# Kernel tuning notes

Measured on AMD Instinct MI355X. Metric: run time of the kernel, lower is better.

The kernel has to match this reference:

```python
import jax, jax.numpy as jnp
import numpy as np

B, IN = 8192, 8000
C, S, O = 16, 500, 64          # num_chunks, chunk_size, fc_repr_dim
F = C * O                       # fc_0_out_feat = 1024
E, D, T = 8, 512, 2            # num_experts, fc_task_dim, num_tasks
NC = (32, 2)                    # num_classes per task
EPS = 1e-5


def _bn(h, g, b, axis):
    # training-mode BatchNorm1d: biased variance over the batch axis
    m = h.mean(axis=axis, keepdims=True)
    v = h.var(axis=axis, keepdims=True)
    return (h - m) * jax.lax.rsqrt(v + EPS) * g + b


def _swish(x):
    return x * jax.nn.sigmoid(x)


def setup_inputs() -> dict:
    key = jax.random.key(0)
    ks = jax.random.split(key, 10)
    s = 0.02
    return {
        "x": jax.random.normal(ks[0], (B, IN), dtype=jnp.float32),
        "w0": jax.random.normal(ks[1], (C, O, S), dtype=jnp.float32) * s,
        "b0": jnp.zeros((F,), jnp.float32),
        "bn0_g": jnp.ones((F,), jnp.float32),
        "bn0_b": jnp.zeros((F,), jnp.float32),
        "gate_w": jax.random.normal(ks[2], (T, F, E), dtype=jnp.float32) * s,
        "gate_b": jnp.zeros((T, E), jnp.float32),
        "exp_w": jax.random.normal(ks[3], (E, F, D), dtype=jnp.float32) * s,
        "exp_bn_g": jnp.ones((E, D), jnp.float32),
        "exp_bn_b": jnp.zeros((E, D), jnp.float32),
        "task_w": jax.random.normal(ks[4], (T, D, D), dtype=jnp.float32) * s,
        "task_bn_g": jnp.ones((T, D), jnp.float32),
        "task_bn_b": jnp.zeros((T, D), jnp.float32),
        "fin_w_a": jax.random.normal(ks[5], (D, NC[0]), dtype=jnp.float32) * s,
        "fin_b_a": jnp.zeros((NC[0],), jnp.float32),
        "fin_w_b": jax.random.normal(ks[6], (D, NC[1]), dtype=jnp.float32) * s,
        "fin_b_b": jnp.zeros((NC[1],), jnp.float32),
    }


def reference(x, w0, b0, bn0_g, bn0_b, gate_w, gate_b, exp_w, exp_bn_g,
              exp_bn_b, task_w, task_bn_g, task_bn_b, fin_w_a, fin_b_a,
              fin_w_b, fin_b_b):
    b = x.shape[0]
    # SplitLinear: block-diagonal linear over C chunks of size S -> O each
    h0 = jnp.einsum('bcs,cos->bco', x.reshape(b, C, S), w0).reshape(b, F) + b0
    h0 = _swish(_bn(h0, bn0_g, bn0_b, axis=0))                  # [B, F]
    # per-task gates with softmax over experts
    gates = jax.nn.softmax(
        jnp.einsum('bf,tfe->tbe', h0, gate_w) + gate_b[:, None, :], axis=-1)
    # expert branches: Linear(no bias) + BN + Swish, vectorized over experts
    eh = jnp.einsum('bf,efd->bed', h0, exp_w)                   # [B, E, D]
    eh = _swish(_bn(eh, exp_bn_g, exp_bn_b, axis=0))
    # gate-weighted sum over experts, per task
    mix = jnp.einsum('tbe,bed->tbd', gates, eh)                 # [T, B, D]
    # task branches: Linear(no bias) + BN + Swish
    th = jnp.einsum('tbd,tdk->tbk', mix, task_w)
    th = _swish(_bn(th, task_bn_g[:, None, :], task_bn_b[:, None, :], axis=1))
    out_a = th[0] @ fin_w_a + fin_b_a                           # [B, 32]
    out_b = th[1] @ fin_w_b + fin_b_b                           # [B, 2]
    return jnp.concatenate([out_a, out_b], axis=1)             # [B, 34]
```

## Files before the change

kernel.cpp:

```cpp
#include <hip/hip_runtime.h>
#include <math.h>

#define B_ 8192
#define IN_ 8000
#define C_ 16
#define S_ 500
#define O_ 64
#define F_ 1024
#define E_ 8
#define D_ 512
#define T_ 2
#define OUTW 34
#define EPS_ 1e-5f

typedef __attribute__((ext_vector_type(8))) short bf16x8;
typedef __attribute__((ext_vector_type(4))) float f32x4;

__device__ __forceinline__ float swishf(float x) {
    return x / (1.0f + __expf(-x));
}

__device__ __forceinline__ unsigned short f2bf(float f) {
    union { float f; unsigned u; } c;
    c.f = f;
    unsigned r = c.u + 0x7fffu + ((c.u >> 16) & 1u);
    return (unsigned short)(r >> 16);
}
__device__ __forceinline__ float bf2f(unsigned short b) {
    union { unsigned u; float f; } c;
    c.u = ((unsigned)b) << 16;
    return c.f;
}

__device__ __forceinline__ void gld16(const void* g, void* l) {
    __builtin_amdgcn_global_load_lds(
        (const __attribute__((address_space(1))) void*)g,
        (__attribute__((address_space(3))) void*)l, 16, 0, 0);
}

__global__ __launch_bounds__(256) void k_split(const float* __restrict__ x,
                                               const float* __restrict__ w0,
                                               const float* __restrict__ b0,
                                               unsigned short* __restrict__ h0raw,
                                               float* __restrict__ psum,
                                               float* __restrict__ psq) {
    __shared__ __align__(16) unsigned short As[128 * 72];
    __shared__ __align__(16) unsigned short Bs[64 * 72];
    int tid = threadIdx.x;
    int c = blockIdx.y;
    int brow0 = blockIdx.x * 128;
    const float* xp = x + (size_t)brow0 * IN_ + c * S_;
    const float* wp = w0 + (size_t)c * O_ * S_;

    int w = tid >> 6, lane = tid & 63;
    int l15 = lane & 15, quad = lane >> 4;
    int wm = w * 32;

    f32x4 acc[2][4] = {};

    for (int k0 = 0; k0 < 512; k0 += 64) {
#pragma unroll
        for (int i = 0; i < 8; i++) {
            int li = tid + i * 256;
            int row = li >> 4, c4 = li & 15;
            int gk = k0 + c4 * 4;
            float4 v = make_float4(0.f, 0.f, 0.f, 0.f);
            if (gk + 3 < S_) v = *(const float4*)(xp + (size_t)row * IN_ + gk);
            unsigned short u[4] = { f2bf(v.x), f2bf(v.y), f2bf(v.z), f2bf(v.w) };
            *(ushort4*)&As[row * 72 + c4 * 4] = *(ushort4*)u;
        }
#pragma unroll
        for (int i = 0; i < 4; i++) {
            int li = tid + i * 256;
            int row = li >> 4, c4 = li & 15;
            int gk = k0 + c4 * 4;
            float4 v = make_float4(0.f, 0.f, 0.f, 0.f);
            if (gk + 3 < S_) v = *(const float4*)(wp + (size_t)row * S_ + gk);
            unsigned short u[4] = { f2bf(v.x), f2bf(v.y), f2bf(v.z), f2bf(v.w) };
            *(ushort4*)&Bs[row * 72 + c4 * 4] = *(ushort4*)u;
        }
        __syncthreads();
#pragma unroll
        for (int kk = 0; kk < 64; kk += 32) {
            bf16x8 af[2], wf[4];
#pragma unroll
            for (int i = 0; i < 2; i++)
                af[i] = *(const bf16x8*)&As[(wm + i * 16 + l15) * 72 + kk + quad * 8];
#pragma unroll
            for (int j = 0; j < 4; j++)
                wf[j] = *(const bf16x8*)&Bs[(j * 16 + l15) * 72 + kk + quad * 8];
#pragma unroll
            for (int i = 0; i < 2; i++)
#pragma unroll
                for (int j = 0; j < 4; j++)
                    acc[i][j] = __builtin_amdgcn_mfma_f32_16x16x32_bf16(af[i], wf[j], acc[i][j], 0, 0, 0);
        }
        __syncthreads();
    }

    int colbase = c * O_;
    float sj[4], qj[4];
#pragma unroll
    for (int j = 0; j < 4; j++) {
        int col = j * 16 + l15;
        float bb = b0[colbase + col];
        float s = 0.f, q = 0.f;
#pragma unroll
        for (int i = 0; i < 2; i++) {
#pragma unroll
            for (int reg = 0; reg < 4; reg++) {
                float v = acc[i][j][reg] + bb;
                int rl = wm + i * 16 + quad * 4 + reg;
                h0raw[(size_t)(brow0 + rl) * F_ + colbase + col] = f2bf(v);
                s += v; q += v * v;
            }
        }
        s += __shfl_down(s, 32, 64); s += __shfl_down(s, 16, 64);
        q += __shfl_down(q, 32, 64); q += __shfl_down(q, 16, 64);
        sj[j] = s; qj[j] = q;
    }
    __syncthreads();
    float* red = (float*)As;
    if (lane < 16) {
#pragma unroll
        for (int j = 0; j < 4; j++) {
            int col = j * 16 + l15;
            red[col * 4 + w] = sj[j];
            red[256 + col * 4 + w] = qj[j];
        }
    }
    __syncthreads();
    if (tid < 64) {
        float ss = red[tid * 4] + red[tid * 4 + 1] + red[tid * 4 + 2] + red[tid * 4 + 3];
        float qq = red[256 + tid * 4] + red[256 + tid * 4 + 1] + red[256 + tid * 4 + 2] + red[256 + tid * 4 + 3];
        size_t idx = (size_t)blockIdx.x * F_ + colbase + tid;
        psum[idx] = ss; psq[idx] = qq;
    }
}

__global__ __launch_bounds__(64) void k_stats_b(const float* __restrict__ psum,
                                                const float* __restrict__ psq,
                                                int N, int YS,
                                                const float* __restrict__ g,
                                                const float* __restrict__ beta,
                                                unsigned long long gslab,
                                                float* __restrict__ scale,
                                                float* __restrict__ shift,
                                                unsigned long long oslab) {
    int n = blockIdx.x * 64 + threadIdx.x;
    int z = blockIdx.z;
    float s = 0.f, q = 0.f;
    for (int y = 0; y < YS; y++) {
        size_t idx = ((size_t)(z * YS + y)) * N + n;
        s += psum[idx]; q += psq[idx];
    }
    float mean = s * (1.0f / B_);
    float var = q * (1.0f / B_) - mean * mean;
    float sc = g[z * gslab + n] * rsqrtf(var + EPS_);
    scale[z * oslab + n] = sc;
    shift[z * oslab + n] = beta[z * gslab + n] - mean * sc;
}

__global__ __launch_bounds__(256) void k_wt2(const float* __restrict__ exp_w,
                                             unsigned short* __restrict__ wtE,
                                             const float* __restrict__ task_w,
                                             unsigned short* __restrict__ twt) {
    int z = blockIdx.z;
    const float* ip; unsigned short* op; int K, N;
    if (z < 8) {
        K = F_; N = D_;
        ip = exp_w + (size_t)z * K * N;
        op = wtE + (size_t)z * N * K;
    } else {
        if (blockIdx.x >= 16) return;
        K = D_; N = D_;
        int zz = z - 8;
        ip = task_w + (size_t)zz * K * N;
        op = twt + (size_t)zz * N * K;
    }
    __shared__ float t[32][33];
    int k0 = blockIdx.x * 32, n0 = blockIdx.y * 32;
    int tn = threadIdx.x & 31, tk = threadIdx.x >> 5;
#pragma unroll
    for (int p = 0; p < 4; p++) {
        int k = tk + p * 8;
        t[k][tn] = ip[(size_t)(k0 + k) * N + n0 + tn];
    }
    __syncthreads();
    int tk2 = threadIdx.x & 31, tn2 = threadIdx.x >> 5;
#pragma unroll
    for (int p = 0; p < 4; p++) {
        int n = tn2 + p * 8;
        op[(size_t)(n0 + n) * K + k0 + tk2] = f2bf(t[tk2][n]);
    }
}

__global__ __launch_bounds__(512) void k_bng(const unsigned short* __restrict__ h0,
                                             const float* __restrict__ scale,
                                             const float* __restrict__ shift,
                                             const float* __restrict__ gate_w,
                                             const float* __restrict__ gate_b,
                                             unsigned short* __restrict__ h0bf,
                                             float* __restrict__ gates) {
    __shared__ __align__(16) unsigned short gwt[16 * 1032];
    __shared__ __align__(16) unsigned short As[32 * 1032];
    __shared__ float plog[4][32][16];
    int tid = threadIdx.x;
    int brow = blockIdx.x * 32;
    for (int idx = tid; idx < 16 * 1024; idx += 512) {
        int col = idx >> 10, f = idx & 1023;
        int t = col >> 3, e = col & 7;
        gwt[col * 1032 + f] = f2bf(gate_w[(size_t)t * (F_ * E_) + (size_t)f * E_ + e]);
    }
    int f0 = (tid & 255) * 4;
    int rh = tid >> 8;
    float4 sc4 = *(const float4*)(scale + f0);
    float4 sh4 = *(const float4*)(shift + f0);
    float scv[4] = { sc4.x, sc4.y, sc4.z, sc4.w };
    float shv[4] = { sh4.x, sh4.y, sh4.z, sh4.w };
#pragma unroll
    for (int r = 0; r < 16; r++) {
        int row = rh * 16 + r;
        ushort4 u = *(const ushort4*)(h0 + (size_t)(brow + row) * F_ + f0);
        unsigned short uu[4] = { u.x, u.y, u.z, u.w };
        unsigned short ov[4];
#pragma unroll
        for (int j = 0; j < 4; j++)
            ov[j] = f2bf(swishf(scv[j] * bf2f(uu[j]) + shv[j]));
        *(ushort4*)(h0bf + (size_t)(brow + row) * F_ + f0) = *(ushort4*)ov;
        *(ushort4*)&As[row * 1032 + f0] = *(ushort4*)ov;
    }
    __syncthreads();
    int w = tid >> 6, lane = tid & 63;
    int l15 = lane & 15, quad = lane >> 4;
    int slot = w & 1, kq = w >> 1;
    f32x4 acc = {};
    const unsigned short* ap = &As[(slot * 16 + l15) * 1032 + kq * 256 + quad * 8];
    const unsigned short* wp = &gwt[l15 * 1032 + kq * 256 + quad * 8];
#pragma unroll
    for (int k0 = 0; k0 < 256; k0 += 32) {
        bf16x8 af = *(const bf16x8*)(ap + k0);
        bf16x8 wf = *(const bf16x8*)(wp + k0);
        acc = __builtin_amdgcn_mfma_f32_16x16x32_bf16(af, wf, acc, 0, 0, 0);
    }
#pragma unroll
    for (int reg = 0; reg < 4; reg++)
        plog[kq][slot * 16 + quad * 4 + reg][l15] = acc[reg];
    __syncthreads();
    if (tid < 32) {
        int r = tid;
        float lg[16];
#pragma unroll
        for (int c = 0; c < 16; c++)
            lg[c] = plog[0][r][c] + plog[1][r][c] + plog[2][r][c] + plog[3][r][c] + gate_b[c];
#pragma unroll
        for (int t = 0; t < 2; t++) {
            float mx = -1e30f;
#pragma unroll
            for (int e = 0; e < 8; e++) mx = fmaxf(mx, lg[t * 8 + e]);
            float ex[8], s = 0.f;
#pragma unroll
            for (int e = 0; e < 8; e++) { ex[e] = __expf(lg[t * 8 + e] - mx); s += ex[e]; }
            float inv = 1.0f / s;
#pragma unroll
            for (int e = 0; e < 8; e++)
                gates[(size_t)t * (B_ * E_) + (size_t)(brow + r) * E_ + e] = ex[e] * inv;
        }
    }
}

__global__ __launch_bounds__(256) void k_gemm_bf16(const unsigned short* __restrict__ A,
                                                   unsigned long long aslab,
                                                   const unsigned short* __restrict__ Wt,
                                                   unsigned long long wslab,
                                                   unsigned short* __restrict__ C,
                                                   unsigned long long cslab, int K,
                                                   float* __restrict__ psum,
                                                   float* __restrict__ psq) {
    __shared__ __align__(16) unsigned short As[128 * 32];
    __shared__ __align__(16) unsigned short Ws[128 * 32];
    int z = blockIdx.z;
    A  += (size_t)z * aslab;
    Wt += (size_t)z * wslab;
    C  += (size_t)z * cslab;
    const int N = gridDim.y * 128;
    int row0 = blockIdx.x * 128, col0 = blockIdx.y * 128;
    int tid = threadIdx.x;
    int w = tid >> 6, lane = tid & 63;
    int l15 = lane & 15, quad = lane >> 4;

    const unsigned short* ga0 = A  + (size_t)(row0 + w * 32 + (lane >> 2)) * K + (lane & 3) * 8;
    const unsigned short* ga1 = ga0 + 16 * (size_t)K;
    const unsigned short* gw0 = Wt + (size_t)(col0 + w * 32 + (lane >> 2)) * K + (lane & 3) * 8;
    const unsigned short* gw1 = gw0 + 16 * (size_t)K;
    unsigned short* la0 = As + (w * 32) * 32;
    unsigned short* la1 = As + (w * 32 + 16) * 32;
    unsigned short* lw0 = Ws + (w * 32) * 32;
    unsigned short* lw1 = Ws + (w * 32 + 16) * 32;

    int wm = (w & 1) * 64, wn = (w >> 1) * 64;
    const unsigned short* Afr = As + (size_t)(wm + l15) * 32 + quad * 8;
    const unsigned short* Wfr = Ws + (size_t)(wn + l15) * 32 + quad * 8;

    f32x4 acc[4][4] = {};

    for (int k0 = 0; k0 < K; k0 += 32) {
        gld16(ga0 + k0, la0);
        gld16(ga1 + k0, la1);
        gld16(gw0 + k0, lw0);
        gld16(gw1 + k0, lw1);
        __syncthreads();
        bf16x8 af[4], wf[4];
#pragma unroll
        for (int i = 0; i < 4; i++) af[i] = *(const bf16x8*)(Afr + i * 16 * 32);
#pragma unroll
        for (int j = 0; j < 4; j++) wf[j] = *(const bf16x8*)(Wfr + j * 16 * 32);
#pragma unroll
        for (int i = 0; i < 4; i++)
#pragma unroll
            for (int j = 0; j < 4; j++)
                acc[i][j] = __builtin_amdgcn_mfma_f32_16x16x32_bf16(af[i], wf[j], acc[i][j], 0, 0, 0);
        __syncthreads();
    }

#pragma unroll
    for (int i = 0; i < 4; i++) {
        int r = row0 + wm + i * 16 + quad * 4;
#pragma unroll
        for (int j = 0; j < 4; j++) {
            int cc = col0 + wn + j * 16 + l15;
            unsigned short* cp = C + (size_t)r * N + cc;
#pragma unroll
            for (int reg = 0; reg < 4; reg++)
                cp[(size_t)reg * N] = f2bf(acc[i][j][reg]);
        }
    }

    float* red = (float*)As;
    float sj[4], qj[4];
#pragma unroll
    for (int j = 0; j < 4; j++) {
        float s = 0.f, q = 0.f;
#pragma unroll
        for (int i = 0; i < 4; i++)
#pragma unroll
            for (int reg = 0; reg < 4; reg++) {
                float v = acc[i][j][reg];
                s += v; q += v * v;
            }
        s += __shfl_down(s, 32, 64); s += __shfl_down(s, 16, 64);
        q += __shfl_down(q, 32, 64); q += __shfl_down(q, 16, 64);
        sj[j] = s; qj[j] = q;
    }
    if (lane < 16) {
#pragma unroll
        for (int j = 0; j < 4; j++) {
            int cib = wn + j * 16 + lane;
            red[cib * 2 + (w & 1)] = sj[j];
            red[256 + cib * 2 + (w & 1)] = qj[j];
        }
    }
    __syncthreads();
    if (tid < 128) {
        float s = red[tid * 2] + red[tid * 2 + 1];
        float q = red[256 + tid * 2] + red[256 + tid * 2 + 1];
        size_t row = (size_t)z * gridDim.x + blockIdx.x;
        psum[row * N + col0 + tid] = s;
        psq[row * N + col0 + tid] = q;
    }
}

__global__ __launch_bounds__(512, 2) void k_gemm256(const unsigned short* __restrict__ A,
                                                    const unsigned short* __restrict__ Wt,
                                                    unsigned short* __restrict__ Cc,
                                                    int N, int K,
                                                    float* __restrict__ psum,
                                                    float* __restrict__ psq) {
    __shared__ __align__(16) unsigned short lds[2][2][2][8192];
    int tid = threadIdx.x;
    int w = tid >> 6, lane = tid & 63;
    int l15 = lane & 15, quad = lane >> 4;
    int wm = w >> 2, wn = w & 3;

    int lin = blockIdx.y * gridDim.x + blockIdx.x;
    int cpx = (gridDim.x * gridDim.y) >> 3;
    int swz = (lin & 7) * cpx + (lin >> 3);
    int bx = swz & (gridDim.x - 1), by = swz / gridDim.x;
    int row0 = bx * 256, col0 = by * 256;

    int srow = tid >> 3, sperm = (tid & 7) ^ (srow & 7);
    const unsigned short* pA = A  + (size_t)(row0 + srow) * K + sperm * 8;
    const unsigned short* pB = Wt + (size_t)(col0 + srow) * K + sperm * 8;

    int aoffs[2];
#pragma unroll
    for (int kk = 0; kk < 2; kk++)
        aoffs[kk] = l15 * 64 + ((kk * 4 + quad) ^ (l15 & 7)) * 8;

    f32x4 acc[8][4] = {};
    bf16x8 afr[4][2], bfr[2][2];
    int nt = K >> 6;

#define STAGE256(t1, nb) do {                                                              \
    const unsigned short* sA = pA + (size_t)(t1) * 64;                                     \
    const unsigned short* sB = pB + (size_t)(t1) * 64;                                     \
    _Pragma("unroll")                                                                      \
    for (int h = 0; h < 2; h++)                                                            \
        _Pragma("unroll")                                                                  \
        for (int L = 0; L < 2; L++) {                                                      \
            gld16(sA + (size_t)(h * 128 + L * 64) * K, &lds[nb][0][h][w * 512 + L * 4096]);\
            gld16(sB + (size_t)(h * 128 + L * 64) * K, &lds[nb][1][h][w * 512 + L * 4096]);\
        }                                                                                  \
} while (0)

#define LDA256(mh) do {                                                                    \
    _Pragma("unroll")                                                                      \
    for (int mf = 0; mf < 4; mf++)                                                         \
        _Pragma("unroll")                                                                  \
        for (int kk = 0; kk < 2; kk++)                                                     \
            afr[mf][kk] = *(const bf16x8*)(Ab + ((mh) * 4 + mf) * 1024 + aoffs[kk]);       \
} while (0)

#define LDB256(nh) do {                                                                    \
    _Pragma("unroll")                                                                      \
    for (int nf = 0; nf < 2; nf++)                                                         \
        _Pragma("unroll")                                                                  \
        for (int kk = 0; kk < 2; kk++)                                                     \
            bfr[nf][kk] = *(const bf16x8*)(Bb + ((nh) * 2 + nf) * 1024 + aoffs[kk]);       \
} while (0)

#define MMA256(mh, nh) do {                                                                \
    _Pragma("unroll")                                                                      \
    for (int mf = 0; mf < 4; mf++)                                                         \
        _Pragma("unroll")                                                                  \
        for (int nf = 0; nf < 2; nf++)                                                     \
            _Pragma("unroll")                                                              \
            for (int kk = 0; kk < 2; kk++)                                                 \
                acc[(mh) * 4 + mf][(nh) * 2 + nf] = __builtin_amdgcn_mfma_f32_16x16x32_bf16(\
                    afr[mf][kk], bfr[nf][kk], acc[(mh) * 4 + mf][(nh) * 2 + nf], 0, 0, 0); \
} while (0)

#define PHASE_MID()                                                                        \
    __builtin_amdgcn_s_barrier();                                                          \
    asm volatile("s_waitcnt lgkmcnt(0)" ::: "memory");                                     \
    __builtin_amdgcn_sched_barrier(0);                                                     \
    __builtin_amdgcn_s_setprio(1);

#define PHASE_END()                                                                        \
    __builtin_amdgcn_s_setprio(0);                                                         \
    __builtin_amdgcn_sched_barrier(0);                                                     \
    __builtin_amdgcn_s_barrier();

    STAGE256(0, 0);
    asm volatile("s_waitcnt vmcnt(0)" ::: "memory");
    __builtin_amdgcn_s_barrier();

    for (int t = 0; t < nt; t++) {
        int buf = t & 1;
        const unsigned short* Ab = &lds[buf][0][wm][0];
        const unsigned short* Bb = &lds[buf][1][wn >> 1][(wn & 1) * 4096];
        LDA256(0); LDB256(0);
        if (t + 1 < nt) STAGE256(t + 1, buf ^ 1);
        PHASE_MID();
        MMA256(0, 0);
        PHASE_END();
        LDB256(1);
        PHASE_MID();
        MMA256(0, 1);
        PHASE_END();
        LDA256(1);
        PHASE_MID();
        MMA256(1, 1);
        PHASE_END();
        LDB256(0);
        PHASE_MID();
        MMA256(1, 0);
        __builtin_amdgcn_s_setprio(0);
        __builtin_amdgcn_sched_barrier(0);
        asm volatile("s_waitcnt vmcnt(0)" ::: "memory");
        __builtin_amdgcn_s_barrier();
    }
#undef STAGE256
#undef LDA256
#undef LDB256
#undef MMA256
#undef PHASE_MID
#undef PHASE_END

    __syncthreads();

#pragma unroll
    for (int mf = 0; mf < 8; mf++) {
        int r = row0 + wm * 128 + mf * 16 + quad * 4;
#pragma unroll
        for (int nf = 0; nf < 4; nf++) {
            int cc = col0 + wn * 64 + nf * 16 + l15;
            unsigned short* cp = Cc + (size_t)r * N + cc;
#pragma unroll
            for (int reg = 0; reg < 4; reg++)
                cp[(size_t)reg * N] = f2bf(acc[mf][nf][reg]);
        }
    }

    float* red = (float*)&lds[0][0][0][0];
    float* redq = red + 512;
    float sj[4], qj[4];
#pragma unroll
    for (int nf = 0; nf < 4; nf++) {
        float s = 0.f, q = 0.f;
#pragma unroll
        for (int mf = 0; mf < 8; mf++)
#pragma unroll
            for (int reg = 0; reg < 4; reg++) {
                float v = acc[mf][nf][reg];
                s += v; q += v * v;
            }
        s += __shfl_down(s, 32, 64); s += __shfl_down(s, 16, 64);
        q += __shfl_down(q, 32, 64); q += __shfl_down(q, 16, 64);
        sj[nf] = s; qj[nf] = q;
    }
    if (quad == 0) {
#pragma unroll
        for (int nf = 0; nf < 4; nf++) {
            int cib = wn * 64 + nf * 16 + l15;
            red[cib * 2 + wm] = sj[nf];
            redq[cib * 2 + wm] = qj[nf];
        }
    }
    __syncthreads();
    if (tid < 256) {
        float s = red[tid * 2] + red[tid * 2 + 1];
        float q = redq[tid * 2] + redq[tid * 2 + 1];
        psum[(size_t)bx * N + col0 + tid] = s;
        psq [(size_t)bx * N + col0 + tid] = q;
    }
}

__global__ __launch_bounds__(256) void k_mix(const unsigned short* __restrict__ eh,
                                             const float* __restrict__ scale,
                                             const float* __restrict__ shift,
                                             const float* __restrict__ gates,
                                             unsigned short* __restrict__ mix) {
    __shared__ float scl[E_ * D_], shl[E_ * D_];
    __shared__ float gl[2][2][8];
    int tid = threadIdx.x;
#pragma unroll
    for (int i = 0; i < 4; i++) {
        int li = tid + i * 256;
        ((float4*)scl)[li] = ((const float4*)scale)[li];
        ((float4*)shl)[li] = ((const float4*)shift)[li];
    }
    if (tid < 32) {
        int sub = tid >> 4, t = (tid >> 3) & 1, e = tid & 7;
        gl[sub][t][e] = gates[(size_t)t * (B_ * E_) + (size_t)(blockIdx.x * 2 + sub) * E_ + e];
    }
    __syncthreads();
    int sub = tid >> 7;
    int b = blockIdx.x * 2 + sub;
    int d0 = (tid & 127) * 4;
    float a0[4] = {0.f, 0.f, 0.f, 0.f}, a1[4] = {0.f, 0.f, 0.f, 0.f};
#pragma unroll
    for (int e = 0; e < E_; e++) {
        ushort4 u = *(const ushort4*)&eh[(size_t)b * (E_ * D_) + e * D_ + d0];
        float4 sc4 = *(const float4*)&scl[e * D_ + d0];
        float4 sh4 = *(const float4*)&shl[e * D_ + d0];
        float g0 = gl[sub][0][e], g1 = gl[sub][1][e];
        unsigned short uu[4] = { u.x, u.y, u.z, u.w };
        float scv[4] = { sc4.x, sc4.y, sc4.z, sc4.w };
        float shv[4] = { sh4.x, sh4.y, sh4.z, sh4.w };
#pragma unroll
        for (int l = 0; l < 4; l++) {
            float sw = swishf(scv[l] * bf2f(uu[l]) + shv[l]);
            a0[l] += g0 * sw;
            a1[l] += g1 * sw;
        }
    }
    unsigned short o0[4], o1[4];
#pragma unroll
    for (int l = 0; l < 4; l++) { o0[l] = f2bf(a0[l]); o1[l] = f2bf(a1[l]); }
    *(ushort4*)&mix[(size_t)b * D_ + d0] = *(ushort4*)o0;
    *(ushort4*)&mix[(size_t)(B_ * D_) + (size_t)b * D_ + d0] = *(ushort4*)o1;
}

__global__ __launch_bounds__(256) void k_final(const unsigned short* __restrict__ th,
                                               const float* __restrict__ scale,
                                               const float* __restrict__ shift,
                                               const float* __restrict__ fwa,
                                               const float* __restrict__ fba,
                                               const float* __restrict__ fwb,
                                               const float* __restrict__ fbb,
                                               float* __restrict__ out) {
    __shared__ float t0[8][D_], t1[8][D_];
    __shared__ float pb[64];
    int tid = threadIdx.x;
    int b0 = blockIdx.x * 8;
#pragma unroll
    for (int t = 0; t < 2; t++) {
#pragma unroll
        for (int i = 0; i < 4; i++) {
            int li = tid + i * 256;
            int row = li >> 7, d = (li & 127) * 4;
            ushort4 u = *(const ushort4*)&th[((size_t)t * B_ + b0 + row) * D_ + d];
            unsigned short uu[4] = { u.x, u.y, u.z, u.w };
            float* dst = t ? &t1[row][d] : &t0[row][d];
#pragma unroll
            for (int l = 0; l < 4; l++)
                dst[l] = swishf(scale[t * D_ + d + l] * bf2f(uu[l]) + shift[t * D_ + d + l]);
        }
    }
    __syncthreads();
    {
        int row = tid >> 5, col = tid & 31;
        float acc = fba[col];
        for (int d = 0; d < D_; d++) acc += t0[row][d] * fwa[d * 32 + col];
        out[(size_t)(b0 + row) * OUTW + col] = acc;
    }
    if (tid < 64) {
        int row = tid >> 3, colb = (tid >> 2) & 1, part = tid & 3;
        float a = 0.f;
        for (int d = part * 128; d < part * 128 + 128; d++) a += t1[row][d] * fwb[d * 2 + colb];
        pb[tid] = a;
    }
    __syncthreads();
    if (tid < 16) {
        int row = tid >> 1, colb = tid & 1;
        int base = row * 8 + colb * 4;
        float a = fbb[colb] + pb[base] + pb[base + 1] + pb[base + 2] + pb[base + 3];
        out[(size_t)(b0 + row) * OUTW + 32 + colb] = a;
    }
}

extern "C" void kernel_launch(void* const* d_in, const int* in_sizes, int n_in,
                              void* d_out, int out_size, void* d_ws, size_t ws_size,
                              hipStream_t stream) {
    const float* x        = (const float*)d_in[0];
    const float* w0       = (const float*)d_in[1];
    const float* b0       = (const float*)d_in[2];
    const float* bn0_g    = (const float*)d_in[3];
    const float* bn0_b    = (const float*)d_in[4];
    const float* gate_w   = (const float*)d_in[5];
    const float* gate_b   = (const float*)d_in[6];
    const float* exp_w    = (const float*)d_in[7];
    const float* exp_bn_g = (const float*)d_in[8];
    const float* exp_bn_b = (const float*)d_in[9];
    const float* task_w   = (const float*)d_in[10];
    const float* task_bn_g= (const float*)d_in[11];
    const float* task_bn_b= (const float*)d_in[12];
    const float* fwa      = (const float*)d_in[13];
    const float* fba      = (const float*)d_in[14];
    const float* fwb      = (const float*)d_in[15];
    const float* fbb      = (const float*)d_in[16];
    float* out = (float*)d_out;

    float* ws = (float*)d_ws;
    unsigned short* ehbf  = (unsigned short*)ws;
    unsigned short* h0raw = (unsigned short*)(ws + 16777216);
    unsigned short* thbf  = ehbf;
    unsigned short* mixbf = h0raw;
    unsigned short* h0bf  = (unsigned short*)(ws + 20971520);
    unsigned short* wtE   = (unsigned short*)(ws + 25165824);
    unsigned short* twt   = (unsigned short*)(ws + 27262976);
    float* gates = ws + 27525120;
    float* sc0   = ws + 27656192;
    float* sh0   = sc0 + 1024;
    float* scE   = sh0 + 1024;
    float* shE   = scE + 4096;
    float* scT   = shE + 4096;
    float* shT   = scT + 1024;
    float* psum  = shT + 1024;
    float* psq   = psum + 262144;

    k_wt2<<<dim3(32, 16, 10), 256, 0, stream>>>(exp_w, wtE, task_w, twt);
    k_split<<<dim3(64, 16), 256, 0, stream>>>(x, w0, b0, h0raw, psum, psq);
    k_stats_b<<<dim3(16, 1, 1), 64, 0, stream>>>(psum, psq, F_, 64, bn0_g, bn0_b, 0ull, sc0, sh0, 0ull);
    k_bng<<<dim3(256), 512, 0, stream>>>(h0raw, sc0, sh0, gate_w, gate_b, h0bf, gates);
    k_gemm256<<<dim3(32, 16), 512, 0, stream>>>(h0bf, wtE, ehbf, E_ * D_, F_, psum, psq);
    k_stats_b<<<dim3(64, 1, 1), 64, 0, stream>>>(psum, psq, E_ * D_, 32, exp_bn_g, exp_bn_b, 0ull, scE, shE, 0ull);
    k_mix<<<dim3(B_ / 2), 256, 0, stream>>>(ehbf, scE, shE, gates, mixbf);
    k_gemm_bf16<<<dim3(64, 4, 2), 256, 0, stream>>>(mixbf, (unsigned long long)(B_ * D_),
                                                    twt, (unsigned long long)(D_ * D_),
                                                    thbf, (unsigned long long)(B_ * D_), D_,
                                                    psum, psq);
    k_stats_b<<<dim3(8, 1, 2), 64, 0, stream>>>(psum, psq, D_, 64, task_bn_g, task_bn_b, 512ull, scT, shT, 512ull);
    k_final<<<dim3(B_ / 8), 256, 0, stream>>>(thbf, scT, shT, fwa, fba, fwb, fbb, out);
}
```

Measured before the change: 638.7 us.

## Fold BN stats kernels into producers and merge weight transpose into split kernel

Removes the three separate k_stats_b launches. BN0 scale and shift are now computed at the start of k_bng. Expert and task BN statistics are accumulated with atomics, and the last finishing block of each GEMM computes scale and shift, using a counter that k_pre resets. The weight transpose kernel is merged into the split GEMM launch as extra blocks. This cuts launch count and serial gaps, at the cost of atomic contention and a last-block pattern that depends on memory fences for correctness.

```diff
diff --git a/kernel.cpp b/kernel.cpp
--- a/kernel.cpp
+++ b/kernel.cpp
@@ -38,17 +38,58 @@
         (__attribute__((address_space(3))) void*)l, 16, 0, 0);
 }
 
-__global__ __launch_bounds__(256) void k_split(const float* __restrict__ x,
-                                               const float* __restrict__ w0,
-                                               const float* __restrict__ b0,
-                                               unsigned short* __restrict__ h0raw,
-                                               float* __restrict__ psum,
-                                               float* __restrict__ psq) {
+__global__ __launch_bounds__(256) void k_pre(const float* __restrict__ x,
+                                             const float* __restrict__ w0,
+                                             const float* __restrict__ b0,
+                                             unsigned short* __restrict__ h0raw,
+                                             float* __restrict__ psum,
+                                             float* __restrict__ psq,
+                                             const float* __restrict__ exp_w,
+                                             unsigned short* __restrict__ wtE,
+                                             const float* __restrict__ task_w,
+                                             unsigned short* __restrict__ twt,
+                                             unsigned* __restrict__ ctrs) {
     __shared__ __align__(16) unsigned short As[128 * 72];
     __shared__ __align__(16) unsigned short Bs[64 * 72];
+    __shared__ float tt[32][33];
     int tid = threadIdx.x;
-    int c = blockIdx.y;
-    int brow0 = blockIdx.x * 128;
+    int bid = blockIdx.x;
+
+    if (bid >= 1024) {
+        int wid = bid - 1024;
+        if (wid == 0 && tid == 0) { ctrs[0] = 0u; ctrs[1] = 0u; }
+        const float* ip; unsigned short* op; int K, N, k0, n0;
+        if (wid < 4096) {
+            int xx = wid & 31, yy = (wid >> 5) & 15, z = wid >> 9;
+            K = F_; N = D_;
+            ip = exp_w + (size_t)z * K * N;
+            op = wtE + (size_t)z * N * K;
+            k0 = xx * 32; n0 = yy * 32;
+        } else {
+            int w2 = wid - 4096;
+            int xx = w2 & 15, yy = (w2 >> 4) & 15, z = w2 >> 8;
+            K = D_; N = D_;
+            ip = task_w + (size_t)z * K * N;
+            op = twt + (size_t)z * N * K;
+            k0 = xx * 32; n0 = yy * 32;
+        }
+        int tn = tid & 31, tk = tid >> 5;
+#pragma unroll
+        for (int p = 0; p < 4; p++) {
+            int k = tk + p * 8;
+            tt[k][tn] = ip[(size_t)(k0 + k) * N + n0 + tn];
+        }
+        __syncthreads();
+#pragma unroll
+        for (int p = 0; p < 4; p++) {
+            int n = tk + p * 8;
+            op[(size_t)(n0 + n) * K + k0 + tn] = f2bf(tt[tn][n]);
+        }
+        return;
+    }
+
+    int bx = bid & 63, c = bid >> 6;
+    int brow0 = bx * 128;
     const float* xp = x + (size_t)brow0 * IN_ + c * S_;
     const float* wp = w0 + (size_t)c * O_ * S_;
 
@@ -133,89 +174,57 @@
     if (tid < 64) {
         float ss = red[tid * 4] + red[tid * 4 + 1] + red[tid * 4 + 2] + red[tid * 4 + 3];
         float qq = red[256 + tid * 4] + red[256 + tid * 4 + 1] + red[256 + tid * 4 + 2] + red[256 + tid * 4 + 3];
-        size_t idx = (size_t)blockIdx.x * F_ + colbase + tid;
+        size_t idx = (size_t)bx * F_ + colbase + tid;
         psum[idx] = ss; psq[idx] = qq;
     }
 }
 
-__global__ __launch_bounds__(64) void k_stats_b(const float* __restrict__ psum,
-                                                const float* __restrict__ psq,
-                                                int N, int YS,
-                                                const float* __restrict__ g,
-                                                const float* __restrict__ beta,
-                                                unsigned long long gslab,
-                                                float* __restrict__ scale,
-                                                float* __restrict__ shift,
-                                                unsigned long long oslab) {
-    int n = blockIdx.x * 64 + threadIdx.x;
-    int z = blockIdx.z;
-    float s = 0.f, q = 0.f;
-    for (int y = 0; y < YS; y++) {
-        size_t idx = ((size_t)(z * YS + y)) * N + n;
-        s += psum[idx]; q += psq[idx];
-    }
-    float mean = s * (1.0f / B_);
-    float var = q * (1.0f / B_) - mean * mean;
-    float sc = g[z * gslab + n] * rsqrtf(var + EPS_);
-    scale[z * oslab + n] = sc;
-    shift[z * oslab + n] = beta[z * gslab + n] - mean * sc;
-}
-
-__global__ __launch_bounds__(256) void k_wt2(const float* __restrict__ exp_w,
-                                             unsigned short* __restrict__ wtE,
-                                             const float* __restrict__ task_w,
-                                             unsigned short* __restrict__ twt) {
-    int z = blockIdx.z;
-    const float* ip; unsigned short* op; int K, N;
-    if (z < 8) {
-        K = F_; N = D_;
-        ip = exp_w + (size_t)z * K * N;
-        op = wtE + (size_t)z * N * K;
-    } else {
-        if (blockIdx.x >= 16) return;
-        K = D_; N = D_;
-        int zz = z - 8;
-        ip = task_w + (size_t)zz * K * N;
-        op = twt + (size_t)zz * N * K;
-    }
-    __shared__ float t[32][33];
-    int k0 = blockIdx.x * 32, n0 = blockIdx.y * 32;
-    int tn = threadIdx.x & 31, tk = threadIdx.x >> 5;
-#pragma unroll
-    for (int p = 0; p < 4; p++) {
-        int k = tk + p * 8;
-        t[k][tn] = ip[(size_t)(k0 + k) * N + n0 + tn];
-    }
-    __syncthreads();
-    int tk2 = threadIdx.x & 31, tn2 = threadIdx.x >> 5;
-#pragma unroll
-    for (int p = 0; p < 4; p++) {
-        int n = tn2 + p * 8;
-        op[(size_t)(n0 + n) * K + k0 + tk2] = f2bf(t[tk2][n]);
-    }
-}
-
 __global__ __launch_bounds__(512) void k_bng(const unsigned short* __restrict__ h0,
-                                             const float* __restrict__ scale,
-                                             const float* __restrict__ shift,
+                                             const float* __restrict__ psum,
+                                             const float* __restrict__ psq,
+                                             const float* __restrict__ bn0_g,
+                                             const float* __restrict__ bn0_b,
                                              const float* __restrict__ gate_w,
                                              const float* __restrict__ gate_b,
                                              unsigned short* __restrict__ h0bf,
-                                             float* __restrict__ gates) {
+                                             float* __restrict__ gates,
+                                             float* __restrict__ psumE,
+                                             float* __restrict__ psqE) {
     __shared__ __align__(16) unsigned short gwt[16 * 1032];
     __shared__ __align__(16) unsigned short As[32 * 1032];
     __shared__ float plog[4][32][16];
+    __shared__ __align__(16) float lsc[1024], lsh[1024];
     int tid = threadIdx.x;
     int brow = blockIdx.x * 32;
+    if (blockIdx.x == 0) {
+        for (int i = tid; i < 4096; i += 512) { psumE[i] = 0.f; psqE[i] = 0.f; }
+    }
     for (int idx = tid; idx < 16 * 1024; idx += 512) {
         int col = idx >> 10, f = idx & 1023;
         int t = col >> 3, e = col & 7;
         gwt[col * 1032 + f] = f2bf(gate_w[(size_t)t * (F_ * E_) + (size_t)f * E_ + e]);
     }
+    {
+        int col = tid * 2;
+        float s0 = 0.f, s1 = 0.f, q0 = 0.f, q1 = 0.f;
+        for (int y = 0; y < 64; y++) {
+            float2 pv = *(const float2*)(psum + (size_t)y * F_ + col);
+            float2 qv = *(const float2*)(psq + (size_t)y * F_ + col);
+            s0 += pv.x; s1 += pv.y; q0 += qv.x; q1 += qv.y;
+        }
+        float m0 = s0 * (1.0f / B_), m1 = s1 * (1.0f / B_);
+        float v0 = q0 * (1.0f / B_) - m0 * m0;
+        float v1 = q1 * (1.0f / B_) - m1 * m1;
+        float c0 = bn0_g[col] * rsqrtf(v0 + EPS_);
+        float c1 = bn0_g[col + 1] * rsqrtf(v1 + EPS_);
+        lsc[col] = c0;     lsh[col] = bn0_b[col] - m0 * c0;
+        lsc[col + 1] = c1; lsh[col + 1] = bn0_b[col + 1] - m1 * c1;
+    }
+    __syncthreads();
     int f0 = (tid & 255) * 4;
     int rh = tid >> 8;
-    float4 sc4 = *(const float4*)(scale + f0);
-    float4 sh4 = *(const float4*)(shift + f0);
+    float4 sc4 = *(const float4*)&lsc[f0];
+    float4 sh4 = *(const float4*)&lsh[f0];
     float scv[4] = { sc4.x, sc4.y, sc4.z, sc4.w };
     float shv[4] = { sh4.x, sh4.y, sh4.z, sh4.w };
 #pragma unroll
@@ -269,113 +278,17 @@
     }
 }
 
-__global__ __launch_bounds__(256) void k_gemm_bf16(const unsigned short* __restrict__ A,
-                                                   unsigned long long aslab,
-                                                   const unsigned short* __restrict__ Wt,
-                                                   unsigned long long wslab,
-                                                   unsigned short* __restrict__ C,
-                                                   unsigned long long cslab, int K,
-                                                   float* __restrict__ psum,
-                                                   float* __restrict__ psq) {
-    __shared__ __align__(16) unsigned short As[128 * 32];
-    __shared__ __align__(16) unsigned short Ws[128 * 32];
-    int z = blockIdx.z;
-    A  += (size_t)z * aslab;
-    Wt += (size_t)z * wslab;
-    C  += (size_t)z * cslab;
-    const int N = gridDim.y * 128;
-    int row0 = blockIdx.x * 128, col0 = blockIdx.y * 128;
-    int tid = threadIdx.x;
-    int w = tid >> 6, lane = tid & 63;
-    int l15 = lane & 15, quad = lane >> 4;
-
-    const unsigned short* ga0 = A  + (size_t)(row0 + w * 32 + (lane >> 2)) * K + (lane & 3) * 8;
-    const unsigned short* ga1 = ga0 + 16 * (size_t)K;
-    const unsigned short* gw0 = Wt + (size_t)(col0 + w * 32 + (lane >> 2)) * K + (lane & 3) * 8;
-    const unsigned short* gw1 = gw0 + 16 * (size_t)K;
-    unsigned short* la0 = As + (w * 32) * 32;
-    unsigned short* la1 = As + (w * 32 + 16) * 32;
-    unsigned short* lw0 = Ws + (w * 32) * 32;
-    unsigned short* lw1 = Ws + (w * 32 + 16) * 32;
-
-    int wm = (w & 1) * 64, wn = (w >> 1) * 64;
-    const unsigned short* Afr = As + (size_t)(wm + l15) * 32 + quad * 8;
-    const unsigned short* Wfr = Ws + (size_t)(wn + l15) * 32 + quad * 8;
-
-    f32x4 acc[4][4] = {};
-
-    for (int k0 = 0; k0 < K; k0 += 32) {
-        gld16(ga0 + k0, la0);
-        gld16(ga1 + k0, la1);
-        gld16(gw0 + k0, lw0);
-        gld16(gw1 + k0, lw1);
-        __syncthreads();
-        bf16x8 af[4], wf[4];
-#pragma unroll
-        for (int i = 0; i < 4; i++) af[i] = *(const bf16x8*)(Afr + i * 16 * 32);
-#pragma unroll
-        for (int j = 0; j < 4; j++) wf[j] = *(const bf16x8*)(Wfr + j * 16 * 32);
-#pragma unroll
-        for (int i = 0; i < 4; i++)
-#pragma unroll
-            for (int j = 0; j < 4; j++)
-                acc[i][j] = __builtin_amdgcn_mfma_f32_16x16x32_bf16(af[i], wf[j], acc[i][j], 0, 0, 0);
-        __syncthreads();
-    }
-
-#pragma unroll
-    for (int i = 0; i < 4; i++) {
-        int r = row0 + wm + i * 16 + quad * 4;
-#pragma unroll
-        for (int j = 0; j < 4; j++) {
-            int cc = col0 + wn + j * 16 + l15;
-            unsigned short* cp = C + (size_t)r * N + cc;
-#pragma unroll
-            for (int reg = 0; reg < 4; reg++)
-                cp[(size_t)reg * N] = f2bf(acc[i][j][reg]);
-        }
-    }
-
-    float* red = (float*)As;
-    float sj[4], qj[4];
-#pragma unroll
-    for (int j = 0; j < 4; j++) {
-        float s = 0.f, q = 0.f;
-#pragma unroll
-        for (int i = 0; i < 4; i++)
-#pragma unroll
-            for (int reg = 0; reg < 4; reg++) {
-                float v = acc[i][j][reg];
-                s += v; q += v * v;
-            }
-        s += __shfl_down(s, 32, 64); s += __shfl_down(s, 16, 64);
-        q += __shfl_down(q, 32, 64); q += __shfl_down(q, 16, 64);
-        sj[j] = s; qj[j] = q;
-    }
-    if (lane < 16) {
-#pragma unroll
-        for (int j = 0; j < 4; j++) {
-            int cib = wn + j * 16 + lane;
-            red[cib * 2 + (w & 1)] = sj[j];
-            red[256 + cib * 2 + (w & 1)] = qj[j];
-        }
-    }
-    __syncthreads();
-    if (tid < 128) {
-        float s = red[tid * 2] + red[tid * 2 + 1];
-        float q = red[256 + tid * 2] + red[256 + tid * 2 + 1];
-        size_t row = (size_t)z * gridDim.x + blockIdx.x;
-        psum[row * N + col0 + tid] = s;
-        psq[row * N + col0 + tid] = q;
-    }
-}
-
 __global__ __launch_bounds__(512, 2) void k_gemm256(const unsigned short* __restrict__ A,
                                                     const unsigned short* __restrict__ Wt,
                                                     unsigned short* __restrict__ Cc,
                                                     int N, int K,
-                                                    float* __restrict__ psum,
-                                                    float* __restrict__ psq) {
+                                                    float* __restrict__ psumE,
+                                                    float* __restrict__ psqE,
+                                                    const float* __restrict__ ebg,
+                                                    const float* __restrict__ ebb,
+                                                    float* __restrict__ scE,
+                                                    float* __restrict__ shE,
+                                                    unsigned* __restrict__ ctr) {
     __shared__ __align__(16) unsigned short lds[2][2][2][8192];
     int tid = threadIdx.x;
     int w = tid >> 6, lane = tid & 63;
@@ -531,8 +444,28 @@
     if (tid < 256) {
         float s = red[tid * 2] + red[tid * 2 + 1];
         float q = redq[tid * 2] + redq[tid * 2 + 1];
-        psum[(size_t)bx * N + col0 + tid] = s;
-        psq [(size_t)bx * N + col0 + tid] = q;
+        atomicAdd(&psumE[col0 + tid], s);
+        atomicAdd(&psqE[col0 + tid], q);
+    }
+
+    __shared__ int amLast;
+    __syncthreads();
+    if (tid == 0) {
+        __threadfence();
+        unsigned old = atomicAdd(ctr, 1u);
+        amLast = (old == (unsigned)(gridDim.x * gridDim.y - 1));
+    }
+    __syncthreads();
+    if (amLast) {
+        __threadfence();
+        for (int n = tid; n < 4096; n += 512) {
+            float s = psumE[n], q = psqE[n];
+            float mean = s * (1.0f / B_);
+            float var = q * (1.0f / B_) - mean * mean;
+            float sc = ebg[n] * rsqrtf(var + EPS_);
+            scE[n] = sc;
+            shE[n] = ebb[n] - mean * sc;
+        }
     }
 }
 
@@ -540,10 +473,15 @@
                                              const float* __restrict__ scale,
                                              const float* __restrict__ shift,
                                              const float* __restrict__ gates,
-                                             unsigned short* __restrict__ mix) {
+                                             unsigned short* __restrict__ mix,
+                                             float* __restrict__ psumT,
+                                             float* __restrict__ psqT) {
     __shared__ float scl[E_ * D_], shl[E_ * D_];
     __shared__ float gl[2][2][8];
     int tid = threadIdx.x;
+    if (blockIdx.x == 0) {
+        for (int i = tid; i < 1024; i += 256) { psumT[i] = 0.f; psqT[i] = 0.f; }
+    }
 #pragma unroll
     for (int i = 0; i < 4; i++) {
         int li = tid + i * 256;
@@ -580,6 +518,131 @@
     for (int l = 0; l < 4; l++) { o0[l] = f2bf(a0[l]); o1[l] = f2bf(a1[l]); }
     *(ushort4*)&mix[(size_t)b * D_ + d0] = *(ushort4*)o0;
     *(ushort4*)&mix[(size_t)(B_ * D_) + (size_t)b * D_ + d0] = *(ushort4*)o1;
+}
+
+__global__ __launch_bounds__(256) void k_gemm_bf16(const unsigned short* __restrict__ A,
+                                                   unsigned long long aslab,
+                                                   const unsigned short* __restrict__ Wt,
+                                                   unsigned long long wslab,
+                                                   unsigned short* __restrict__ C,
+                                                   unsigned long long cslab, int K,
+                                                   float* __restrict__ psumT,
+                                                   float* __restrict__ psqT,
+                                                   const float* __restrict__ tbg,
+                                                   const float* __restrict__ tbb,
+                                                   float* __restrict__ scT,
+                                                   float* __restrict__ shT,
+                                                   unsigned* __restrict__ ctr) {
+    __shared__ __align__(16) unsigned short As[128 * 32];
+    __shared__ __align__(16) unsigned short Ws[128 * 32];
+    int z = blockIdx.z;
+    A  += (size_t)z * aslab;
+    Wt += (size_t)z * wslab;
+    C  += (size_t)z * cslab;
+    const int N = gridDim.y * 128;
+    int row0 = blockIdx.x * 128, col0 = blockIdx.y * 128;
+    int tid = threadIdx.x;
+    int w = tid >> 6, lane = tid & 63;
+    int l15 = lane & 15, quad = lane >> 4;
+
+    const unsigned short* ga0 = A  + (size_t)(row0 + w * 32 + (lane >> 2)) * K + (lane & 3) * 8;
+    const unsigned short* ga1 = ga0 + 16 * (size_t)K;
+    const unsigned short* gw0 = Wt + (size_t)(col0 + w * 32 + (lane >> 2)) * K + (lane & 3) * 8;
+    const unsigned short* gw1 = gw0 + 16 * (size_t)K;
+    unsigned short* la0 = As + (w * 32) * 32;
+    unsigned short* la1 = As + (w * 32 + 16) * 32;
+    unsigned short* lw0 = Ws + (w * 32) * 32;
+    unsigned short* lw1 = Ws + (w * 32 + 16) * 32;
+
+    int wm = (w & 1) * 64, wn = (w >> 1) * 64;
+    const unsigned short* Afr = As + (size_t)(wm + l15) * 32 + quad * 8;
+    const unsigned short* Wfr = Ws + (size_t)(wn + l15) * 32 + quad * 8;
+
+    f32x4 acc[4][4] = {};
+
+    for (int k0 = 0; k0 < K; k0 += 32) {
+        gld16(ga0 + k0, la0);
+        gld16(ga1 + k0, la1);
+        gld16(gw0 + k0, lw0);
+        gld16(gw1 + k0, lw1);
+        __syncthreads();
+        bf16x8 af[4], wf[4];
+#pragma unroll
+        for (int i = 0; i < 4; i++) af[i] = *(const bf16x8*)(Afr + i * 16 * 32);
+#pragma unroll
+        for (int j = 0; j < 4; j++) wf[j] = *(const bf16x8*)(Wfr + j * 16 * 32);
+#pragma unroll
+        for (int i = 0; i < 4; i++)
+#pragma unroll
+            for (int j = 0; j < 4; j++)
+                acc[i][j] = __builtin_amdgcn_mfma_f32_16x16x32_bf16(af[i], wf[j], acc[i][j], 0, 0, 0);
+        __syncthreads();
+    }
+
+#pragma unroll
+    for (int i = 0; i < 4; i++) {
+        int r = row0 + wm + i * 16 + quad * 4;
+#pragma unroll
+        for (int j = 0; j < 4; j++) {
+            int cc = col0 + wn + j * 16 + l15;
+            unsigned short* cp = C + (size_t)r * N + cc;
+#pragma unroll
+            for (int reg = 0; reg < 4; reg++)
+                cp[(size_t)reg * N] = f2bf(acc[i][j][reg]);
+        }
+    }
+
+    float* red = (float*)As;
+    float sj[4], qj[4];
+#pragma unroll
+    for (int j = 0; j < 4; j++) {
+        float s = 0.f, q = 0.f;
+#pragma unroll
+        for (int i = 0; i < 4; i++)
+#pragma unroll
+            for (int reg = 0; reg < 4; reg++) {
+                float v = acc[i][j][reg];
+                s += v; q += v * v;
+            }
+        s += __shfl_down(s, 32, 64); s += __shfl_down(s, 16, 64);
+        q += __shfl_down(q, 32, 64); q += __shfl_down(q, 16, 64);
+        sj[j] = s; qj[j] = q;
+    }
+    if (lane < 16) {
+#pragma unroll
+        for (int j = 0; j < 4; j++) {
+            int cib = wn + j * 16 + lane;
+            red[cib * 2 + (w & 1)] = sj[j];
+            red[256 + cib * 2 + (w & 1)] = qj[j];
+        }
+    }
+    __syncthreads();
+    if (tid < 128) {
+        float s = red[tid * 2] + red[tid * 2 + 1];
+        float q = red[256 + tid * 2] + red[256 + tid * 2 + 1];
+        atomicAdd(&psumT[(size_t)z * 512 + col0 + tid], s);
+        atomicAdd(&psqT[(size_t)z * 512 + col0 + tid], q);
+    }
+
+    __shared__ int amLast;
+    __syncthreads();
+    if (tid == 0) {
+        __threadfence();
+        unsigned old = atomicAdd(ctr, 1u);
+        amLast = (old == (unsigned)(gridDim.x * gridDim.y * gridDim.z - 1));
+    }
+    __syncthreads();
+    if (amLast) {
+        __threadfence();
+        for (int idx = tid; idx < 1024; idx += 256) {
+            float s = psumT[idx], q = psqT[idx];
+            float mean = s * (1.0f / B_);
+            float var = q * (1.0f / B_) - mean * mean;
+            float sc = tbg[idx] * rsqrtf(var + EPS_);
+            scT[idx] = sc;
+            shT[idx] = tbb[idx] - mean * sc;
+        }
+    }
 }
 
 __global__ __launch_bounds__(256) void k_final(const unsigned short* __restrict__ th,
@@ -661,26 +724,30 @@
     unsigned short* wtE   = (unsigned short*)(ws + 25165824);
     unsigned short* twt   = (unsigned short*)(ws + 27262976);
     float* gates = ws + 27525120;
-    float* sc0   = ws + 27656192;
-    float* sh0   = sc0 + 1024;
-    float* scE   = sh0 + 1024;
+    float* scE   = ws + 27656192;
     float* shE   = scE + 4096;
     float* scT   = shE + 4096;
     float* shT   = scT + 1024;
     float* psum  = shT + 1024;
-    float* psq   = psum + 262144;
-
-    k_wt2<<<dim3(32, 16, 10), 256, 0, stream>>>(exp_w, wtE, task_w, twt);
-    k_split<<<dim3(64, 16), 256, 0, stream>>>(x, w0, b0, h0raw, psum, psq);
-    k_stats_b<<<dim3(16, 1, 1), 64, 0, stream>>>(psum, psq, F_, 64, bn0_g, bn0_b, 0ull, sc0, sh0, 0ull);
-    k_bng<<<dim3(256), 512, 0, stream>>>(h0raw, sc0, sh0, gate_w, gate_b, h0bf, gates);
-    k_gemm256<<<dim3(32, 16), 512, 0, stream>>>(h0bf, wtE, ehbf, E_ * D_, F_, psum, psq);
-    k_stats_b<<<dim3(64, 1, 1), 64, 0, stream>>>(psum, psq, E_ * D_, 32, exp_bn_g, exp_bn_b, 0ull, scE, shE, 0ull);
-    k_mix<<<dim3(B_ / 2), 256, 0, stream>>>(ehbf, scE, shE, gates, mixbf);
+    float* psq   = psum + 65536;
+    float* psumE = psq + 65536;
+    float* psqE  = psumE + 4096;
+    float* psumT = psqE + 4096;
+    float* psqT  = psumT + 1024;
+    unsigned* ctrs = (unsigned*)(psqT + 1024);
+
+    k_pre<<<dim3(5632), 256, 0, stream>>>(x, w0, b0, h0raw, psum, psq,
+                                          exp_w, wtE, task_w, twt, ctrs);
+    k_bng<<<dim3(256), 512, 0, stream>>>(h0raw, psum, psq, bn0_g, bn0_b,
+                                         gate_w, gate_b, h0bf, gates, psumE, psqE);
+    k_gemm256<<<dim3(32, 16), 512, 0, stream>>>(h0bf, wtE, ehbf, E_ * D_, F_,
+                                                psumE, psqE, exp_bn_g, exp_bn_b,
+                                                scE, shE, &ctrs[0]);
+    k_mix<<<dim3(B_ / 2), 256, 0, stream>>>(ehbf, scE, shE, gates, mixbf, psumT, psqT);
     k_gemm_bf16<<<dim3(64, 4, 2), 256, 0, stream>>>(mixbf, (unsigned long long)(B_ * D_),
                                                     twt, (unsigned long long)(D_ * D_),
                                                     thbf, (unsigned long long)(B_ * D_), D_,
-                                                    psum, psq);
-    k_stats_b<<<dim3(8, 1, 2), 64, 0, stream>>>(psum, psq, D_, 64, task_bn_g, task_bn_b, 512ull, scT, shT, 512ull);
+                                                    psumT, psqT, task_bn_g, task_bn_b,
+                                                    scT, shT, &ctrs[1]);
     k_final<<<dim3(B_ / 8), 256, 0, stream>>>(thbf, scT, shT, fwa, fba, fwb, fbb, out);
 }
```

New measurement: 631.6 us. Within noise of the previous version (-1.1%).
